# Kernel optimization log

Measured on AMD Instinct MI355X. Metric: run time of the kernel, lower is better.

The kernel has to match this reference:

```python
import jax, jax.numpy as jnp
import numpy as np

NUM_HEADS = 16
SIZE_PER_HEAD = 64
NEG_INF = -10000.0

def setup_inputs() -> dict:
    key = jax.random.key(0)
    ks = jax.random.split(key, 4)
    B, S, D = 4, 2048, 1024
    x = jax.random.normal(ks[0], (B, S, D), dtype=jnp.float32)
    mask = jnp.ones((B, S), dtype=jnp.int32)
    std = 0.02
    Wq = jax.random.normal(ks[1], (D, NUM_HEADS * SIZE_PER_HEAD), dtype=jnp.float32) * std
    Wk = jax.random.normal(ks[2], (D, NUM_HEADS * SIZE_PER_HEAD), dtype=jnp.float32) * std
    Wv = jax.random.normal(ks[3], (D, NUM_HEADS * SIZE_PER_HEAD), dtype=jnp.float32) * std
    bq = jnp.zeros((NUM_HEADS * SIZE_PER_HEAD,), dtype=jnp.float32)
    bk = jnp.zeros((NUM_HEADS * SIZE_PER_HEAD,), dtype=jnp.float32)
    bv = jnp.zeros((NUM_HEADS * SIZE_PER_HEAD,), dtype=jnp.float32)
    return {"x": x, "mask": mask, "Wq": Wq, "bq": bq, "Wk": Wk, "bk": bk, "Wv": Wv, "bv": bv}

def reference(x, mask, Wq, bq, Wk, bk, Wv, bv):
    B, S, D = x.shape
    H, Dh = NUM_HEADS, SIZE_PER_HEAD
    # QKV projections (no activations: query/key/value_activation default None)
    q = (x @ Wq + bq).reshape(B, S, H, Dh).transpose(0, 2, 1, 3)  # [B,H,S,Dh]
    k = (x @ Wk + bk).reshape(B, S, H, Dh).transpose(0, 2, 1, 3)
    v = (x @ Wv + bv).reshape(B, S, H, Dh).transpose(0, 2, 1, 3)
    scores = jnp.einsum('bhqd,bhkd->bhqk', q, k) / jnp.sqrt(jnp.float32(Dh))  # [B,H,S,S]
    # additive mask: (1 - mask) * neg_inf, broadcast over heads and query dim
    adder = (1.0 - mask.astype(jnp.float32))[:, None, None, :] * NEG_INF
    probs = jax.nn.softmax(scores + adder, axis=-1)
    # dropout is identity at inference (training=None)
    ctx = jnp.einsum('bhqk,bhkd->bhqd', probs, v)  # [B,H,S,Dh]
    return ctx.transpose(0, 2, 1, 3).reshape(B, S, H * Dh)
```

## Files before the change

kernel.cpp:

```cpp
#include <hip/hip_runtime.h>


typedef __attribute__((ext_vector_type(8))) short bf16x8;
typedef __attribute__((ext_vector_type(4))) float f32x4;
typedef __attribute__((ext_vector_type(16))) float f32x16;

#define LOG2E 1.4426950408889634f

__device__ __forceinline__ ushort f2bf(float f) {
  union { float f; unsigned int u; } x; x.f = f;
  unsigned int r = x.u + 0x7fffu + ((x.u >> 16) & 1u);
  return (ushort)(r >> 16);
}

__device__ __forceinline__ void gload16(const ushort* g, ushort* l) {
  __builtin_amdgcn_global_load_lds(
      (__attribute__((address_space(1))) unsigned int*)(g),
      (__attribute__((address_space(3))) unsigned int*)(l), 16, 0, 0);
}

__global__ __launch_bounds__(256) void prep(
    const float* __restrict__ x, ushort* __restrict__ xb,
    const float* __restrict__ Wq, const float* __restrict__ Wk,
    const float* __restrict__ Wv, ushort* __restrict__ WT,
    const int* __restrict__ mask, int* __restrict__ flagw) {
  __shared__ float tile[32][33];
  __shared__ int accum[64];
  const int blk = blockIdx.x, t = threadIdx.x;
  if (blk < 8192) {
    int i = blk * 256 + t;
    float4 v = ((const float4*)x)[i];
    ushort4 o;
    o.x = f2bf(v.x); o.y = f2bf(v.y); o.z = f2bf(v.z); o.w = f2bf(v.w);
    ((ushort4*)xb)[i] = o;
  } else if (blk < 11264) {
    int bb = blk - 8192;
    int z = bb >> 10, rem = bb & 1023, db = rem >> 5, nb = rem & 31;
    const float* W = (z == 0) ? Wq : ((z == 1) ? Wk : Wv);
    int tx = t & 31, ty = t >> 5;
#pragma unroll
    for (int i = 0; i < 4; i++) {
      int dl = ty + i * 8;
      tile[dl][tx] = W[(size_t)(db * 32 + dl) * 1024 + nb * 32 + tx];
    }
    __syncthreads();
#pragma unroll
    for (int i = 0; i < 4; i++) {
      int nl = ty + i * 8;
      WT[(size_t)(z * 1024 + nb * 32 + nl) * 1024 + db * 32 + tx] = f2bf(tile[tx][nl]);
    }
  } else {
    if (t < 64) accum[t] = 0;
    __syncthreads();
    int p = t >> 2, j = t & 3;
    int base = p * 128 + j * 32;
    int s = 0;
#pragma unroll
    for (int i = 0; i < 8; i++) {
      int4 v = *(const int4*)(mask + base + i * 4);
      s += v.x + v.y + v.z + v.w;
    }
    atomicAdd(&accum[p], s);
    __syncthreads();
    if (t < 4) {
      int w = 0;
#pragma unroll
      for (int kt = 0; kt < 16; kt++)
        if (accum[t * 16 + kt] != 128) w |= (1 << kt);
      flagw[t] = w;
    }
  }
}

__global__ __launch_bounds__(256, 2) void gemm_qkv(
    const ushort* __restrict__ xb, const ushort* __restrict__ WT,
    const float* __restrict__ bq, const float* __restrict__ bk,
    const float* __restrict__ bv, ushort* __restrict__ Qg,
    ushort* __restrict__ Kg, ushort* __restrict__ VTg) {
  __shared__ __align__(16) ushort As[128 * 64];
  __shared__ __align__(16) ushort Bs[128 * 64];
  const int t = threadIdx.x, wid = t >> 6, lane = t & 63;
  const int blk = blockIdx.x;
  int mode, mb, nb;
  const ushort *A, *B;
  if (blk < 1024) {
    mode = 0;
    int lin2 = (blk & 7) * 128 + (blk >> 3);
    nb = lin2 & 15; mb = lin2 >> 4;
    A = xb; B = WT;
  } else {
    mode = 1;
    int l = blk - 1024;
    int lin2 = (l & 7) * 64 + (l >> 3);
    mb = lin2 & 7; nb = lin2 >> 3;
    A = WT + (size_t)2048 * 1024; B = xb;
  }
  const ushort* Ab = A + (size_t)mb * 128 * 1024;
  const ushort* Bb = B + (size_t)nb * 128 * 1024;
  const int wr = wid >> 1, wc = wid & 1;

  f32x4 acc[4][4] = {};

  const int srow = lane >> 3;
  const int schunk = (lane & 7) ^ srow;

#pragma unroll
  for (int i = 0; i < 4; i++) {
    int blki = i * 4 + wid;
    int row = blki * 8 + srow;
    int ldso = __builtin_amdgcn_readfirstlane(blki * 512);
    gload16(Ab + (size_t)row * 1024 + schunk * 8, As + ldso);
    gload16(Bb + (size_t)row * 1024 + schunk * 8, Bs + ldso);
  }

  for (int kt = 0; kt < 16; ++kt) {
    __syncthreads();

    bf16x8 af[2][4], bf[2][4];
#pragma unroll
    for (int ks = 0; ks < 2; ks++) {
#pragma unroll
      for (int m = 0; m < 4; m++) {
        int row = wr * 64 + m * 16 + (lane & 15);
        int slot = (ks * 4 + (lane >> 4)) ^ (row & 7);
        af[ks][m] = *(const bf16x8*)(As + row * 64 + slot * 8);
      }
#pragma unroll
      for (int n = 0; n < 4; n++) {
        int row = wc * 64 + n * 16 + (lane & 15);
        int slot = (ks * 4 + (lane >> 4)) ^ (row & 7);
        bf[ks][n] = *(const bf16x8*)(Bs + row * 64 + slot * 8);
      }
    }
    __syncthreads();

    if (kt < 15) {
      const int kof = (kt + 1) * 64 + schunk * 8;
#pragma unroll
      for (int i = 0; i < 4; i++) {
        int blki = i * 4 + wid;
        int row = blki * 8 + srow;
        int ldso = __builtin_amdgcn_readfirstlane(blki * 512);
        gload16(Ab + (size_t)row * 1024 + kof, As + ldso);
        gload16(Bb + (size_t)row * 1024 + kof, Bs + ldso);
      }
    }

#pragma unroll
    for (int ks = 0; ks < 2; ks++)
#pragma unroll
      for (int m = 0; m < 4; m++)
#pragma unroll
        for (int n = 0; n < 4; n++)
          acc[m][n] = __builtin_amdgcn_mfma_f32_16x16x32_bf16(
              af[ks][m], bf[ks][n], acc[m][n], 0, 0, 0);
  }

#pragma unroll
  for (int m = 0; m < 4; m++) {
#pragma unroll
    for (int n = 0; n < 4; n++) {
      if (mode == 0) {
        int col = nb * 128 + wc * 64 + n * 16 + (lane & 15);
        int wq = col >> 10;
        float bs = wq ? bk[col & 1023] : bq[col & 1023];
        float scale = wq ? 1.0f : (0.125f * LOG2E);
        ushort* dst = wq ? Kg : Qg;
        int h = (col >> 6) & 15, d = col & 63;
#pragma unroll
        for (int r = 0; r < 4; r++) {
          int row = mb * 128 + wr * 64 + m * 16 + (lane >> 4) * 4 + r;
          int b = row >> 11, s = row & 2047;
          float v = (acc[m][n][r] + bs) * scale;
          dst[((size_t)((b << 4) + h) * 2048 + s) * 64 + d] = f2bf(v);
        }
      } else {
        int col = nb * 128 + wc * 64 + n * 16 + (lane & 15);
        int b = col >> 11, s = col & 2047;
#pragma unroll
        for (int r = 0; r < 4; r++) {
          int p = mb * 128 + wr * 64 + m * 16 + (lane >> 4) * 4 + r;
          float v = acc[m][n][r] + bv[p];
          int h = p >> 6, d = p & 63;
          VTg[((size_t)((b << 4) + h) * 64 + d) * 2048 + s] = f2bf(v);
        }
      }
    }
  }
}

__global__ __launch_bounds__(256, 3) void attn_kernel(
    const ushort* __restrict__ Qg, const ushort* __restrict__ Kg,
    const ushort* __restrict__ VTg, const int* __restrict__ mask,
    const int* __restrict__ flagw, float* __restrict__ out) {
  __shared__ __align__(16) ushort Ks[128 * 64];
  __shared__ __align__(16) ushort Vs[64 * 128];
  __shared__ float maddv[128];

  const int t = threadIdx.x, wid = t >> 6, lane = t & 63;
  const int l31 = lane & 31, hi = lane >> 5;
  const int lin = blockIdx.x;
  const int lin2 = (lin & 7) * 128 + (lin >> 3);
  const int qb = lin2 & 15, bh = lin2 >> 4;
  const int b = bh >> 4, h = bh & 15;
  const ushort* Qbh = Qg + ((size_t)bh * 2048 + qb * 128) * 64;
  const ushort* Kbh = Kg + (size_t)bh * 2048 * 64;
  const ushort* Vbh = VTg + (size_t)bh * 64 * 2048;

  const int pr_l = lane >> 4;
  const int s_l = lane & 15;
  const int spk = s_l ^ (4 * wid + pr_l);
  const int okl = 128 * pr_l + (spk >> 3) * 64 + (spk & 7) * 8;
  const int ovl = 2048 * pr_l + spk * 8;

  const int prq = l31 >> 1;
  const int hq8 = (l31 & 1) << 3;

#pragma unroll
  for (int i = 0; i < 4; i++) {
    int blki = i * 4 + wid;
    int ldso = __builtin_amdgcn_readfirstlane(blki * 512);
    gload16(Qbh + blki * 512 + okl, Ks + ldso);
  }
  const int fb = flagw[b];
  __syncthreads();
  bf16x8 qf[4];
  {
    const ushort* qbase = Ks + (wid * 16 + prq) * 128;
#pragma unroll
    for (int ds = 0; ds < 4; ds++) {
      int slot = ((ds * 2 + hi) | hq8) ^ prq;
      qf[ds] = *(const bf16x8*)(qbase + slot * 8);
    }
  }
  __syncthreads();

  f32x16 cacc[2] = {};
  float l0 = 0.f, l1 = 0.f;

  for (int kt = 0; kt < 16; ++kt) {
#pragma unroll
    for (int i = 0; i < 4; i++) {
      int blki = i * 4 + wid;
      int ldso = __builtin_amdgcn_readfirstlane(blki * 512);
      gload16(Kbh + kt * 8192 + blki * 512 + okl, Ks + ldso);
      gload16(Vbh + blki * 8192 + kt * 128 + ovl, Vs + ldso);
    }
    const bool msk = ((fb >> kt) & 1) != 0;
    if (msk && t < 128)
      maddv[t] = (1.0f - (float)mask[b * 2048 + kt * 128 + t]) * (-10000.0f * LOG2E);
    __syncthreads();

#pragma unroll
    for (int kb = 0; kb < 4; kb++) {
      const ushort* krow = Ks + (kb * 16 + prq) * 128;
      const f32x16 zz = {};
      __builtin_amdgcn_s_setprio(1);
      bf16x8 kf0 = *(const bf16x8*)(krow + (((0 + hi) | hq8) ^ prq) * 8);
      f32x16 a = __builtin_amdgcn_mfma_f32_32x32x16_bf16(kf0, qf[0], zz, 0, 0, 0);
      bf16x8 kf1 = *(const bf16x8*)(krow + (((2 + hi) | hq8) ^ prq) * 8);
      a = __builtin_amdgcn_mfma_f32_32x32x16_bf16(kf1, qf[1], a, 0, 0, 0);
      bf16x8 kf2 = *(const bf16x8*)(krow + (((4 + hi) | hq8) ^ prq) * 8);
      a = __builtin_amdgcn_mfma_f32_32x32x16_bf16(kf2, qf[2], a, 0, 0, 0);
      bf16x8 kf3 = *(const bf16x8*)(krow + (((6 + hi) | hq8) ^ prq) * 8);
      a = __builtin_amdgcn_mfma_f32_32x32x16_bf16(kf3, qf[3], a, 0, 0, 0);
      __builtin_amdgcn_s_setprio(0);

      if (msk) {
#pragma unroll
        for (int qd = 0; qd < 4; qd++) {
          f32x4 ma = *(const f32x4*)(maddv + kb * 32 + qd * 8 + hi * 4);
#pragma unroll
          for (int rr = 0; rr < 4; rr++) a[qd * 4 + rr] += ma[rr];
        }
      }

#pragma unroll
      for (int w2 = 0; w2 < 2; w2++) {
        const int o = w2 * 8;
        float e0 = __builtin_amdgcn_exp2f(a[o + 0]);
        float e1 = __builtin_amdgcn_exp2f(a[o + 1]);
        float e2 = __builtin_amdgcn_exp2f(a[o + 2]);
        float e3 = __builtin_amdgcn_exp2f(a[o + 3]);
        float e4 = __builtin_amdgcn_exp2f(a[o + 4]);
        float e5 = __builtin_amdgcn_exp2f(a[o + 5]);
        float e6 = __builtin_amdgcn_exp2f(a[o + 6]);
        float e7 = __builtin_amdgcn_exp2f(a[o + 7]);
        l0 += e0; l1 += e1; l0 += e2; l1 += e3;
        l0 += e4; l1 += e5; l0 += e6; l1 += e7;
        unsigned a0, a1, b0, b1;
        asm("v_cvt_pk_bf16_f32 %0, %1, %2" : "=v"(a0) : "v"(e0), "v"(e1));
        asm("v_cvt_pk_bf16_f32 %0, %1, %2" : "=v"(a1) : "v"(e2), "v"(e3));
        asm("v_cvt_pk_bf16_f32 %0, %1, %2" : "=v"(b0) : "v"(e4), "v"(e5));
        asm("v_cvt_pk_bf16_f32 %0, %1, %2" : "=v"(b1) : "v"(e6), "v"(e7));
        asm("v_permlane32_swap_b32 %0, %1" : "+v"(a0), "+v"(b0));
        asm("v_permlane32_swap_b32 %0, %1" : "+v"(a1), "+v"(b1));
        union { unsigned u[4]; bf16x8 v8; } pu;
        pu.u[0] = a0; pu.u[1] = a1; pu.u[2] = b0; pu.u[3] = b1;
        bf16x8 pf = pu.v8;
        int w = kb * 2 + w2;
        __builtin_amdgcn_s_setprio(1);
#pragma unroll
        for (int df = 0; df < 2; df++) {
          int d = df * 32 + l31;
          int c = (w * 2 + hi) ^ (d & 15);
          bf16x8 vf = *(const bf16x8*)(Vs + d * 128 + c * 8);
          cacc[df] = __builtin_amdgcn_mfma_f32_32x32x16_bf16(vf, pf, cacc[df], 0, 0, 0);
        }
        __builtin_amdgcn_s_setprio(0);
      }
    }
    __syncthreads();
  }

  float lrun = l0 + l1;
  lrun += __shfl_xor(lrun, 32);
  float linv = 1.0f / lrun;
  int qg = qb * 128 + wid * 32 + l31;
  float* op = out + ((size_t)(b * 2048 + qg)) * 1024 + h * 64;
#pragma unroll
  for (int df = 0; df < 2; df++)
#pragma unroll
    for (int qd = 0; qd < 4; qd++) {
      f32x4 v;
      v[0] = cacc[df][qd * 4 + 0] * linv;
      v[1] = cacc[df][qd * 4 + 1] * linv;
      v[2] = cacc[df][qd * 4 + 2] * linv;
      v[3] = cacc[df][qd * 4 + 3] * linv;
      *(f32x4*)(op + df * 32 + qd * 8 + hi * 4) = v;
    }
}

extern "C" void kernel_launch(void* const* d_in, const int* in_sizes, int n_in,
                              void* d_out, int out_size, void* d_ws, size_t ws_size,
                              hipStream_t stream) {
  const float* x  = (const float*)d_in[0];
  const int* mask = (const int*)d_in[1];
  const float* Wq = (const float*)d_in[2];
  const float* bq = (const float*)d_in[3];
  const float* Wk = (const float*)d_in[4];
  const float* bk = (const float*)d_in[5];
  const float* Wv = (const float*)d_in[6];
  const float* bv = (const float*)d_in[7];
  float* out = (float*)d_out;

  char* ws = (char*)d_ws;
  ushort* xb  = (ushort*)(ws);
  ushort* WT  = (ushort*)(ws + (size_t)16777216);
  ushort* Qg  = (ushort*)(ws + (size_t)23068672);
  ushort* Kg  = (ushort*)(ws + (size_t)39845888);
  ushort* VTg = (ushort*)(ws + (size_t)56623104);
  int*    flg = (int*)(ws + (size_t)73400320);

  prep<<<dim3(11265), dim3(256), 0, stream>>>(x, xb, Wq, Wk, Wv, WT, mask, flg);
  gemm_qkv<<<dim3(1536), dim3(256), 0, stream>>>(xb, WT, bq, bk, bv, Qg, Kg, VTg);
  attn_kernel<<<dim3(1024), dim3(256), 0, stream>>>(Qg, Kg, VTg, mask, flg, out);
}
```

Before: 155.8 us.

## Read Q, K, V and mask directly from global memory instead of LDS staging

The attention kernel no longer stages Q, K, V tiles and mask adders in shared memory through global_load_lds and barriers. Each lane now loads its MFMA operand fragments straight from global memory (relying on L1/L2 caching) and computes the mask adder inline. This removes LDS traffic and per-tile __syncthreads, but each of the four waves now fetches the same K/V data on its own. It also loses the explicit prefetch overlap, so global load latency sits directly in front of the MFMAs.

```diff
diff --git a/kernel.cpp b/kernel.cpp
--- a/kernel.cpp
+++ b/kernel.cpp
@@ -193,85 +193,61 @@
     const ushort* __restrict__ Qg, const ushort* __restrict__ Kg,
     const ushort* __restrict__ VTg, const int* __restrict__ mask,
     const int* __restrict__ flagw, float* __restrict__ out) {
-  __shared__ __align__(16) ushort Ks[128 * 64];
-  __shared__ __align__(16) ushort Vs[64 * 128];
-  __shared__ float maddv[128];
-
   const int t = threadIdx.x, wid = t >> 6, lane = t & 63;
   const int l31 = lane & 31, hi = lane >> 5;
   const int lin = blockIdx.x;
   const int lin2 = (lin & 7) * 128 + (lin >> 3);
   const int qb = lin2 & 15, bh = lin2 >> 4;
   const int b = bh >> 4, h = bh & 15;
-  const ushort* Qbh = Qg + ((size_t)bh * 2048 + qb * 128) * 64;
   const ushort* Kbh = Kg + (size_t)bh * 2048 * 64;
   const ushort* Vbh = VTg + (size_t)bh * 64 * 2048;
 
-  const int pr_l = lane >> 4;
-  const int s_l = lane & 15;
-  const int spk = s_l ^ (4 * wid + pr_l);
-  const int okl = 128 * pr_l + (spk >> 3) * 64 + (spk & 7) * 8;
-  const int ovl = 2048 * pr_l + spk * 8;
-
-  const int prq = l31 >> 1;
-  const int hq8 = (l31 & 1) << 3;
-
-#pragma unroll
-  for (int i = 0; i < 4; i++) {
-    int blki = i * 4 + wid;
-    int ldso = __builtin_amdgcn_readfirstlane(blki * 512);
-    gload16(Qbh + blki * 512 + okl, Ks + ldso);
-  }
-  const int fb = flagw[b];
-  __syncthreads();
   bf16x8 qf[4];
   {
-    const ushort* qbase = Ks + (wid * 16 + prq) * 128;
-#pragma unroll
-    for (int ds = 0; ds < 4; ds++) {
-      int slot = ((ds * 2 + hi) | hq8) ^ prq;
-      qf[ds] = *(const bf16x8*)(qbase + slot * 8);
-    }
-  }
-  __syncthreads();
+    const ushort* qrow =
+        Qg + ((size_t)bh * 2048 + qb * 128 + wid * 32 + l31) * 64 + hi * 8;
+#pragma unroll
+    for (int ds = 0; ds < 4; ds++)
+      qf[ds] = *(const bf16x8*)(qrow + ds * 16);
+  }
+  const int fb = flagw[b];
+
+  const ushort* kl = Kbh + l31 * 64 + hi * 8;
+  const ushort* vl = Vbh + (size_t)l31 * 2048 + hi * 8;
+  const int* ml = mask + b * 2048 + hi * 4;
 
   f32x16 cacc[2] = {};
   float l0 = 0.f, l1 = 0.f;
 
   for (int kt = 0; kt < 16; ++kt) {
-#pragma unroll
-    for (int i = 0; i < 4; i++) {
-      int blki = i * 4 + wid;
-      int ldso = __builtin_amdgcn_readfirstlane(blki * 512);
-      gload16(Kbh + kt * 8192 + blki * 512 + okl, Ks + ldso);
-      gload16(Vbh + blki * 8192 + kt * 128 + ovl, Vs + ldso);
-    }
+    const ushort* kp = kl + kt * 8192;
+    const ushort* vp = vl + kt * 128;
     const bool msk = ((fb >> kt) & 1) != 0;
-    if (msk && t < 128)
-      maddv[t] = (1.0f - (float)mask[b * 2048 + kt * 128 + t]) * (-10000.0f * LOG2E);
-    __syncthreads();
 
 #pragma unroll
     for (int kb = 0; kb < 4; kb++) {
-      const ushort* krow = Ks + (kb * 16 + prq) * 128;
+      const ushort* kq = kp + kb * 2048;
       const f32x16 zz = {};
       __builtin_amdgcn_s_setprio(1);
-      bf16x8 kf0 = *(const bf16x8*)(krow + (((0 + hi) | hq8) ^ prq) * 8);
+      bf16x8 kf0 = *(const bf16x8*)(kq);
       f32x16 a = __builtin_amdgcn_mfma_f32_32x32x16_bf16(kf0, qf[0], zz, 0, 0, 0);
-      bf16x8 kf1 = *(const bf16x8*)(krow + (((2 + hi) | hq8) ^ prq) * 8);
+      bf16x8 kf1 = *(const bf16x8*)(kq + 16);
       a = __builtin_amdgcn_mfma_f32_32x32x16_bf16(kf1, qf[1], a, 0, 0, 0);
-      bf16x8 kf2 = *(const bf16x8*)(krow + (((4 + hi) | hq8) ^ prq) * 8);
+      bf16x8 kf2 = *(const bf16x8*)(kq + 32);
       a = __builtin_amdgcn_mfma_f32_32x32x16_bf16(kf2, qf[2], a, 0, 0, 0);
-      bf16x8 kf3 = *(const bf16x8*)(krow + (((6 + hi) | hq8) ^ prq) * 8);
+      bf16x8 kf3 = *(const bf16x8*)(kq + 48);
       a = __builtin_amdgcn_mfma_f32_32x32x16_bf16(kf3, qf[3], a, 0, 0, 0);
       __builtin_amdgcn_s_setprio(0);
 
       if (msk) {
+        const int* mb_ = ml + kt * 128 + kb * 32;
 #pragma unroll
         for (int qd = 0; qd < 4; qd++) {
-          f32x4 ma = *(const f32x4*)(maddv + kb * 32 + qd * 8 + hi * 4);
-#pragma unroll
-          for (int rr = 0; rr < 4; rr++) a[qd * 4 + rr] += ma[rr];
+          int4 mv = *(const int4*)(mb_ + qd * 8);
+          a[qd * 4 + 0] += (1.0f - (float)mv.x) * (-10000.0f * LOG2E);
+          a[qd * 4 + 1] += (1.0f - (float)mv.y) * (-10000.0f * LOG2E);
+          a[qd * 4 + 2] += (1.0f - (float)mv.z) * (-10000.0f * LOG2E);
+          a[qd * 4 + 3] += (1.0f - (float)mv.w) * (-10000.0f * LOG2E);
         }
       }
 
@@ -298,19 +274,15 @@
         union { unsigned u[4]; bf16x8 v8; } pu;
         pu.u[0] = a0; pu.u[1] = a1; pu.u[2] = b0; pu.u[3] = b1;
         bf16x8 pf = pu.v8;
-        int w = kb * 2 + w2;
         __builtin_amdgcn_s_setprio(1);
 #pragma unroll
         for (int df = 0; df < 2; df++) {
-          int d = df * 32 + l31;
-          int c = (w * 2 + hi) ^ (d & 15);
-          bf16x8 vf = *(const bf16x8*)(Vs + d * 128 + c * 8);
+          bf16x8 vf = *(const bf16x8*)(vp + df * 65536 + kb * 32 + w2 * 16);
           cacc[df] = __builtin_amdgcn_mfma_f32_32x32x16_bf16(vf, pf, cacc[df], 0, 0, 0);
         }
         __builtin_amdgcn_s_setprio(0);
       }
     }
-    __syncthreads();
   }
 
   float lrun = l0 + l1;
```

Result: slower. 341.5 us (+119.3%).

## Double-buffer K/V tiles in LDS to overlap loads with attention compute

Applied to the files above, without the earlier changes.

Allocates two LDS buffers each for K, V^T and the mask adder, and prefetches tile kt+1 while tile kt is computed. The loop is unrolled by two through a macro and needs only one barrier per tile instead of two. This hides global-to-LDS latency inside each block. In exchange it doubles LDS use to about 65KB per block, which likely cuts resident blocks per CU from three to two.

```diff
diff --git a/kernel.cpp b/kernel.cpp
--- a/kernel.cpp
+++ b/kernel.cpp
@@ -189,13 +189,89 @@
   }
 }
 
+
+#define ATTN_STEP(KT, CUR, NXT)                                                \
+  {                                                                            \
+    if ((KT) < 15) {                                                           \
+      _Pragma("unroll")                                                        \
+      for (int i = 0; i < 4; i++) {                                            \
+        int blki = i * 4 + wid;                                                \
+        int ldso = __builtin_amdgcn_readfirstlane(blki * 512);                 \
+        gload16(Kbh + ((KT) + 1) * 8192 + blki * 512 + okl, &Ks[NXT][0] + ldso); \
+        gload16(Vbh + blki * 8192 + ((KT) + 1) * 128 + ovl, &Vs[NXT][0] + ldso); \
+      }                                                                        \
+      if (((fb >> ((KT) + 1)) & 1) && t < 128)                                 \
+        maddv[NXT][t] = (1.0f - (float)mask[b * 2048 + ((KT) + 1) * 128 + t])  \
+                        * (-10000.0f * LOG2E);                                 \
+    }                                                                          \
+    const bool msk = ((fb >> (KT)) & 1) != 0;                                  \
+    _Pragma("unroll")                                                          \
+    for (int kb = 0; kb < 4; kb++) {                                           \
+      const ushort* krow = &Ks[CUR][0] + (kb * 16 + prq) * 128;                \
+      const f32x16 zz = {};                                                    \
+      __builtin_amdgcn_s_setprio(1);                                           \
+      bf16x8 kf0 = *(const bf16x8*)(krow + (((0 + hi) | hq8) ^ prq) * 8);      \
+      f32x16 a = __builtin_amdgcn_mfma_f32_32x32x16_bf16(kf0, qf[0], zz, 0, 0, 0); \
+      bf16x8 kf1 = *(const bf16x8*)(krow + (((2 + hi) | hq8) ^ prq) * 8);      \
+      a = __builtin_amdgcn_mfma_f32_32x32x16_bf16(kf1, qf[1], a, 0, 0, 0);     \
+      bf16x8 kf2 = *(const bf16x8*)(krow + (((4 + hi) | hq8) ^ prq) * 8);      \
+      a = __builtin_amdgcn_mfma_f32_32x32x16_bf16(kf2, qf[2], a, 0, 0, 0);     \
+      bf16x8 kf3 = *(const bf16x8*)(krow + (((6 + hi) | hq8) ^ prq) * 8);      \
+      a = __builtin_amdgcn_mfma_f32_32x32x16_bf16(kf3, qf[3], a, 0, 0, 0);     \
+      __builtin_amdgcn_s_setprio(0);                                           \
+      if (msk) {                                                               \
+        _Pragma("unroll")                                                      \
+        for (int qd = 0; qd < 4; qd++) {                                       \
+          f32x4 ma = *(const f32x4*)(&maddv[CUR][0] + kb * 32 + qd * 8 + hi * 4); \
+          _Pragma("unroll")                                                    \
+          for (int rr = 0; rr < 4; rr++) a[qd * 4 + rr] += ma[rr];             \
+        }                                                                      \
+      }                                                                        \
+      _Pragma("unroll")                                                        \
+      for (int w2 = 0; w2 < 2; w2++) {                                         \
+        const int o = w2 * 8;                                                  \
+        float e0 = __builtin_amdgcn_exp2f(a[o + 0]);                           \
+        float e1 = __builtin_amdgcn_exp2f(a[o + 1]);                           \
+        float e2 = __builtin_amdgcn_exp2f(a[o + 2]);                           \
+        float e3 = __builtin_amdgcn_exp2f(a[o + 3]);                           \
+        float e4 = __builtin_amdgcn_exp2f(a[o + 4]);                           \
+        float e5 = __builtin_amdgcn_exp2f(a[o + 5]);                           \
+        float e6 = __builtin_amdgcn_exp2f(a[o + 6]);                           \
+        float e7 = __builtin_amdgcn_exp2f(a[o + 7]);                           \
+        l0 += e0; l1 += e1; l0 += e2; l1 += e3;                                \
+        l0 += e4; l1 += e5; l0 += e6; l1 += e7;                                \
+        unsigned a0, a1, b0, b1;                                               \
+        asm("v_cvt_pk_bf16_f32 %0, %1, %2" : "=v"(a0) : "v"(e0), "v"(e1));     \
+        asm("v_cvt_pk_bf16_f32 %0, %1, %2" : "=v"(a1) : "v"(e2), "v"(e3));     \
+        asm("v_cvt_pk_bf16_f32 %0, %1, %2" : "=v"(b0) : "v"(e4), "v"(e5));     \
+        asm("v_cvt_pk_bf16_f32 %0, %1, %2" : "=v"(b1) : "v"(e6), "v"(e7));     \
+        asm("v_permlane32_swap_b32 %0, %1" : "+v"(a0), "+v"(b0));              \
+        asm("v_permlane32_swap_b32 %0, %1" : "+v"(a1), "+v"(b1));              \
+        union { unsigned u[4]; bf16x8 v8; } pu;                                \
+        pu.u[0] = a0; pu.u[1] = a1; pu.u[2] = b0; pu.u[3] = b1;                \
+        bf16x8 pf = pu.v8;                                                     \
+        int w = kb * 2 + w2;                                                   \
+        __builtin_amdgcn_s_setprio(1);                                         \
+        _Pragma("unroll")                                                      \
+        for (int df = 0; df < 2; df++) {                                       \
+          int d = df * 32 + l31;                                               \
+          int c = (w * 2 + hi) ^ (d & 15);                                     \
+          bf16x8 vf = *(const bf16x8*)(&Vs[CUR][0] + d * 128 + c * 8);         \
+          cacc[df] = __builtin_amdgcn_mfma_f32_32x32x16_bf16(vf, pf, cacc[df], 0, 0, 0); \
+        }                                                                      \
+        __builtin_amdgcn_s_setprio(0);                                         \
+      }                                                                        \
+    }                                                                          \
+    if ((KT) < 15) __syncthreads();                                            \
+  }
+
 __global__ __launch_bounds__(256, 3) void attn_kernel(
     const ushort* __restrict__ Qg, const ushort* __restrict__ Kg,
     const ushort* __restrict__ VTg, const int* __restrict__ mask,
     const int* __restrict__ flagw, float* __restrict__ out) {
-  __shared__ __align__(16) ushort Ks[128 * 64];
-  __shared__ __align__(16) ushort Vs[64 * 128];
-  __shared__ float maddv[128];
+  __shared__ __align__(16) ushort Ks[2][128 * 64];
+  __shared__ __align__(16) ushort Vs[2][64 * 128];
+  __shared__ float maddv[2][128];
 
   const int t = threadIdx.x, wid = t >> 6, lane = t & 63;
   const int l31 = lane & 31, hi = lane >> 5;
@@ -220,13 +296,17 @@
   for (int i = 0; i < 4; i++) {
     int blki = i * 4 + wid;
     int ldso = __builtin_amdgcn_readfirstlane(blki * 512);
-    gload16(Qbh + blki * 512 + okl, Ks + ldso);
+    gload16(Qbh + blki * 512 + okl, &Ks[0][0] + ldso);
+    gload16(Kbh + blki * 512 + okl, &Ks[1][0] + ldso);
+    gload16(Vbh + blki * 8192 + ovl, &Vs[1][0] + ldso);
   }
   const int fb = flagw[b];
+  if (((fb >> 0) & 1) && t < 128)
+    maddv[1][t] = (1.0f - (float)mask[b * 2048 + t]) * (-10000.0f * LOG2E);
   __syncthreads();
   bf16x8 qf[4];
   {
-    const ushort* qbase = Ks + (wid * 16 + prq) * 128;
+    const ushort* qbase = &Ks[0][0] + (wid * 16 + prq) * 128;
 #pragma unroll
     for (int ds = 0; ds < 4; ds++) {
       int slot = ((ds * 2 + hi) | hq8) ^ prq;
@@ -238,79 +318,9 @@
   f32x16 cacc[2] = {};
   float l0 = 0.f, l1 = 0.f;
 
-  for (int kt = 0; kt < 16; ++kt) {
-#pragma unroll
-    for (int i = 0; i < 4; i++) {
-      int blki = i * 4 + wid;
-      int ldso = __builtin_amdgcn_readfirstlane(blki * 512);
-      gload16(Kbh + kt * 8192 + blki * 512 + okl, Ks + ldso);
-      gload16(Vbh + blki * 8192 + kt * 128 + ovl, Vs + ldso);
-    }
-    const bool msk = ((fb >> kt) & 1) != 0;
-    if (msk && t < 128)
-      maddv[t] = (1.0f - (float)mask[b * 2048 + kt * 128 + t]) * (-10000.0f * LOG2E);
-    __syncthreads();
-
-#pragma unroll
-    for (int kb = 0; kb < 4; kb++) {
-      const ushort* krow = Ks + (kb * 16 + prq) * 128;
-      const f32x16 zz = {};
-      __builtin_amdgcn_s_setprio(1);
-      bf16x8 kf0 = *(const bf16x8*)(krow + (((0 + hi) | hq8) ^ prq) * 8);
-      f32x16 a = __builtin_amdgcn_mfma_f32_32x32x16_bf16(kf0, qf[0], zz, 0, 0, 0);
-      bf16x8 kf1 = *(const bf16x8*)(krow + (((2 + hi) | hq8) ^ prq) * 8);
-      a = __builtin_amdgcn_mfma_f32_32x32x16_bf16(kf1, qf[1], a, 0, 0, 0);
-      bf16x8 kf2 = *(const bf16x8*)(krow + (((4 + hi) | hq8) ^ prq) * 8);
-      a = __builtin_amdgcn_mfma_f32_32x32x16_bf16(kf2, qf[2], a, 0, 0, 0);
-      bf16x8 kf3 = *(const bf16x8*)(krow + (((6 + hi) | hq8) ^ prq) * 8);
-      a = __builtin_amdgcn_mfma_f32_32x32x16_bf16(kf3, qf[3], a, 0, 0, 0);
-      __builtin_amdgcn_s_setprio(0);
-
-      if (msk) {
-#pragma unroll
-        for (int qd = 0; qd < 4; qd++) {
-          f32x4 ma = *(const f32x4*)(maddv + kb * 32 + qd * 8 + hi * 4);
-#pragma unroll
-          for (int rr = 0; rr < 4; rr++) a[qd * 4 + rr] += ma[rr];
-        }
-      }
-
-#pragma unroll
-      for (int w2 = 0; w2 < 2; w2++) {
-        const int o = w2 * 8;
-        float e0 = __builtin_amdgcn_exp2f(a[o + 0]);
-        float e1 = __builtin_amdgcn_exp2f(a[o + 1]);
-        float e2 = __builtin_amdgcn_exp2f(a[o + 2]);
-        float e3 = __builtin_amdgcn_exp2f(a[o + 3]);
-        float e4 = __builtin_amdgcn_exp2f(a[o + 4]);
-        float e5 = __builtin_amdgcn_exp2f(a[o + 5]);
-        float e6 = __builtin_amdgcn_exp2f(a[o + 6]);
-        float e7 = __builtin_amdgcn_exp2f(a[o + 7]);
-        l0 += e0; l1 += e1; l0 += e2; l1 += e3;
-        l0 += e4; l1 += e5; l0 += e6; l1 += e7;
-        unsigned a0, a1, b0, b1;
-        asm("v_cvt_pk_bf16_f32 %0, %1, %2" : "=v"(a0) : "v"(e0), "v"(e1));
-        asm("v_cvt_pk_bf16_f32 %0, %1, %2" : "=v"(a1) : "v"(e2), "v"(e3));
-        asm("v_cvt_pk_bf16_f32 %0, %1, %2" : "=v"(b0) : "v"(e4), "v"(e5));
-        asm("v_cvt_pk_bf16_f32 %0, %1, %2" : "=v"(b1) : "v"(e6), "v"(e7));
-        asm("v_permlane32_swap_b32 %0, %1" : "+v"(a0), "+v"(b0));
-        asm("v_permlane32_swap_b32 %0, %1" : "+v"(a1), "+v"(b1));
-        union { unsigned u[4]; bf16x8 v8; } pu;
-        pu.u[0] = a0; pu.u[1] = a1; pu.u[2] = b0; pu.u[3] = b1;
-        bf16x8 pf = pu.v8;
-        int w = kb * 2 + w2;
-        __builtin_amdgcn_s_setprio(1);
-#pragma unroll
-        for (int df = 0; df < 2; df++) {
-          int d = df * 32 + l31;
-          int c = (w * 2 + hi) ^ (d & 15);
-          bf16x8 vf = *(const bf16x8*)(Vs + d * 128 + c * 8);
-          cacc[df] = __builtin_amdgcn_mfma_f32_32x32x16_bf16(vf, pf, cacc[df], 0, 0, 0);
-        }
-        __builtin_amdgcn_s_setprio(0);
-      }
-    }
-    __syncthreads();
+  for (int kt2 = 0; kt2 < 16; kt2 += 2) {
+    ATTN_STEP(kt2, 1, 0)
+    ATTN_STEP(kt2 + 1, 0, 1)
   }
 
   float lrun = l0 + l1;
```

New measurement: 164.5 us. 1.06x slower.

## Prefetch next K/V tile into registers while computing current tile

Applied to the files above, without the earlier changes.

Replaces the direct global-to-LDS loads of K and V tiles with register staging. The loads for tile kt+1 are issued before computing on tile kt and written to LDS after a barrier, so global latency overlaps the MFMA work. Occupancy is lowered from 3 to 2 blocks per SM via launch bounds to leave room for the extra staging registers. The risk is fewer resident waves to hide latency, plus an extra LDS write pass through VGPRs.

```diff
diff --git a/kernel.cpp b/kernel.cpp
--- a/kernel.cpp
+++ b/kernel.cpp
@@ -189,7 +189,7 @@
   }
 }
 
-__global__ __launch_bounds__(256, 3) void attn_kernel(
+__global__ __launch_bounds__(256, 2) void attn_kernel(
     const ushort* __restrict__ Qg, const ushort* __restrict__ Kg,
     const ushort* __restrict__ VTg, const int* __restrict__ mask,
     const int* __restrict__ flagw, float* __restrict__ out) {
@@ -212,6 +212,10 @@
   const int spk = s_l ^ (4 * wid + pr_l);
   const int okl = 128 * pr_l + (spk >> 3) * 64 + (spk & 7) * 8;
   const int ovl = 2048 * pr_l + spk * 8;
+  const int lwr = 512 * wid + lane * 8;
+
+  const ushort* Kst = Kbh + 512 * wid + okl;
+  const ushort* Vst = Vbh + 8192 * wid + ovl;
 
   const int prq = l31 >> 1;
   const int hq8 = (l31 & 1) << 3;
@@ -222,6 +226,11 @@
     int ldso = __builtin_amdgcn_readfirstlane(blki * 512);
     gload16(Qbh + blki * 512 + okl, Ks + ldso);
   }
+  bf16x8 kst[4], vst[4];
+#pragma unroll
+  for (int i = 0; i < 4; i++) kst[i] = *(const bf16x8*)(Kst + 2048 * i);
+#pragma unroll
+  for (int i = 0; i < 4; i++) vst[i] = *(const bf16x8*)(Vst + 32768 * i);
   const int fb = flagw[b];
   __syncthreads();
   bf16x8 qf[4];
@@ -234,22 +243,28 @@
     }
   }
   __syncthreads();
+#pragma unroll
+  for (int i = 0; i < 4; i++) *(bf16x8*)(Ks + 2048 * i + lwr) = kst[i];
+#pragma unroll
+  for (int i = 0; i < 4; i++) *(bf16x8*)(Vs + 2048 * i + lwr) = vst[i];
+  if (((fb >> 0) & 1) && t < 128)
+    maddv[t] = (1.0f - (float)mask[b * 2048 + t]) * (-10000.0f * LOG2E);
 
   f32x16 cacc[2] = {};
   float l0 = 0.f, l1 = 0.f;
 
   for (int kt = 0; kt < 16; ++kt) {
-#pragma unroll
-    for (int i = 0; i < 4; i++) {
-      int blki = i * 4 + wid;
-      int ldso = __builtin_amdgcn_readfirstlane(blki * 512);
-      gload16(Kbh + kt * 8192 + blki * 512 + okl, Ks + ldso);
-      gload16(Vbh + blki * 8192 + kt * 128 + ovl, Vs + ldso);
+    __syncthreads();
+
+    if (kt < 15) {
+#pragma unroll
+      for (int i = 0; i < 4; i++)
+        kst[i] = *(const bf16x8*)(Kst + (size_t)(kt + 1) * 8192 + 2048 * i);
+#pragma unroll
+      for (int i = 0; i < 4; i++)
+        vst[i] = *(const bf16x8*)(Vst + 32768 * i + (kt + 1) * 128);
     }
     const bool msk = ((fb >> kt) & 1) != 0;
-    if (msk && t < 128)
-      maddv[t] = (1.0f - (float)mask[b * 2048 + kt * 128 + t]) * (-10000.0f * LOG2E);
-    __syncthreads();
 
 #pragma unroll
     for (int kb = 0; kb < 4; kb++) {
@@ -310,7 +325,16 @@
         __builtin_amdgcn_s_setprio(0);
       }
     }
-    __syncthreads();
+
+    if (kt < 15) {
+      __syncthreads();
+#pragma unroll
+      for (int i = 0; i < 4; i++) *(bf16x8*)(Ks + 2048 * i + lwr) = kst[i];
+#pragma unroll
+      for (int i = 0; i < 4; i++) *(bf16x8*)(Vs + 2048 * i + lwr) = vst[i];
+      if (((fb >> (kt + 1)) & 1) && t < 128)
+        maddv[t] = (1.0f - (float)mask[b * 2048 + (kt + 1) * 128 + t]) * (-10000.0f * LOG2E);
+    }
   }
 
   float lrun = l0 + l1;
```

Measured after the change: 158.9 us. 1.02x slower.
